# Kernel tuning notes

Measured on AMD Instinct MI355X. Metric: run time of the kernel, lower is better.

Reference implementation:

```python
import jax, jax.numpy as jnp
from jax import lax
import numpy as np

INPUT_SIZE = 2
HIDDEN_SIZE = 64
OUTPUT_SIZE = 2
SEQ_LEN = 1024
BATCH = 512


def setup_inputs() -> dict:
    key = jax.random.key(0)
    ks = jax.random.split(key, 7)
    H, I, O = HIDDEN_SIZE, INPUT_SIZE, OUTPUT_SIZE
    s = 1.0 / np.sqrt(H)  # PyTorch LSTM/Linear init scale
    x = jax.random.normal(ks[0], (SEQ_LEN, BATCH, I), dtype=jnp.float32)
    W_ih = jax.random.uniform(ks[1], (4 * H, I), minval=-s, maxval=s, dtype=jnp.float32)
    W_hh = jax.random.uniform(ks[2], (4 * H, H), minval=-s, maxval=s, dtype=jnp.float32)
    b_ih = jax.random.uniform(ks[3], (4 * H,), minval=-s, maxval=s, dtype=jnp.float32)
    b_hh = jax.random.uniform(ks[4], (4 * H,), minval=-s, maxval=s, dtype=jnp.float32)
    W_fc = jax.random.uniform(ks[5], (O, H), minval=-s, maxval=s, dtype=jnp.float32)
    b_fc = jax.random.uniform(ks[6], (O,), minval=-s, maxval=s, dtype=jnp.float32)
    return {"x": x, "W_ih": W_ih, "W_hh": W_hh, "b_ih": b_ih, "b_hh": b_hh,
            "W_fc": W_fc, "b_fc": b_fc}


def reference(x, W_ih, W_hh, b_ih, b_hh, W_fc, b_fc):
    # x: [T, B, I] (torch nn.LSTM default batch_first=False)
    T, B, _ = x.shape
    H = W_hh.shape[1]
    b = b_ih + b_hh  # [4H]

    def step(carry, xt):
        h, c = carry  # [B, H] each
        gates = xt @ W_ih.T + h @ W_hh.T + b  # [B, 4H]
        i, f, g, o = jnp.split(gates, 4, axis=-1)  # PyTorch gate order i,f,g,o
        i = jax.nn.sigmoid(i)
        f = jax.nn.sigmoid(f)
        g = jnp.tanh(g)
        o = jax.nn.sigmoid(o)
        c_new = f * c + i * g
        h_new = o * jnp.tanh(c_new)
        return (h_new, c_new), h_new

    h0 = jnp.zeros((B, H), dtype=x.dtype)
    c0 = jnp.zeros((B, H), dtype=x.dtype)
    _, hs = lax.scan(step, (h0, c0), x)  # hs: [T, B, H]

    # Faithful to torch: out[:, -1, :] with out shape [T, B, H] selects the
    # LAST BATCH element's hidden state at every timestep -> [T, H].
    last = hs[:, -1, :]
    return last @ W_fc.T + b_fc  # [T, O]
```

## Files before the change

kernel.cpp:

```cpp
#include <hip/hip_runtime.h>


typedef float f32x2 __attribute__((ext_vector_type(2)));

#define T_LEN 1024
#define BATCH 512
#define HID   64

__device__ __forceinline__ float fast_rcp(float x) {
    return __builtin_amdgcn_rcpf(x);
}
__device__ __forceinline__ float fast_sigmoid(float x) {
    return fast_rcp(1.0f + __expf(-x));
}
__device__ __forceinline__ float fast_tanh(float x) {
    return 1.0f - 2.0f * fast_rcp(__expf(2.0f * x) + 1.0f);
}

__global__ __launch_bounds__(64, 1)
void lstm_seq_kernel(const float* __restrict__ x,
                     const float* __restrict__ W_ih,
                     const float* __restrict__ W_hh,
                     const float* __restrict__ b_ih,
                     const float* __restrict__ b_hh,
                     const float* __restrict__ W_fc,
                     const float* __restrict__ b_fc,
                     float* __restrict__ out,
                     float* __restrict__ hist)
{
    __shared__ float xs[2 * T_LEN];

    const int lane = threadIdx.x;

    for (int j = 0; j < 16; ++j) {
        const int t = lane + 64 * j;
        const float2 v = *(const float2*)(x + (size_t)(t * BATCH + (BATCH - 1)) * 2);
        xs[2 * t]     = v.x;
        xs[2 * t + 1] = v.y;
    }

    f32x2 w0[32], w1[32], w2[32], w3[32];
    {
        const float4* r0 = (const float4*)(W_hh + (0 * HID + lane) * HID);
        const float4* r1 = (const float4*)(W_hh + (1 * HID + lane) * HID);
        const float4* r2 = (const float4*)(W_hh + (2 * HID + lane) * HID);
        const float4* r3 = (const float4*)(W_hh + (3 * HID + lane) * HID);
        #pragma unroll
        for (int k = 0; k < 16; ++k) {
            float4 v;
            v = r0[k]; w0[2*k] = (f32x2){v.x, v.y}; w0[2*k+1] = (f32x2){v.z, v.w};
            v = r1[k]; w1[2*k] = (f32x2){v.x, v.y}; w1[2*k+1] = (f32x2){v.z, v.w};
            v = r2[k]; w2[2*k] = (f32x2){v.x, v.y}; w2[2*k+1] = (f32x2){v.z, v.w};
            v = r3[k]; w3[2*k] = (f32x2){v.x, v.y}; w3[2*k+1] = (f32x2){v.z, v.w};
        }
    }
    const float wi00 = W_ih[(0 * HID + lane) * 2 + 0], wi01 = W_ih[(0 * HID + lane) * 2 + 1];
    const float wi10 = W_ih[(1 * HID + lane) * 2 + 0], wi11 = W_ih[(1 * HID + lane) * 2 + 1];
    const float wi20 = W_ih[(2 * HID + lane) * 2 + 0], wi21 = W_ih[(2 * HID + lane) * 2 + 1];
    const float wi30 = W_ih[(3 * HID + lane) * 2 + 0], wi31 = W_ih[(3 * HID + lane) * 2 + 1];
    const float bs0 = b_ih[0 * HID + lane] + b_hh[0 * HID + lane];
    const float bs1 = b_ih[1 * HID + lane] + b_hh[1 * HID + lane];
    const float bs2 = b_ih[2 * HID + lane] + b_hh[2 * HID + lane];
    const float bs3 = b_ih[3 * HID + lane] + b_hh[3 * HID + lane];

    float hval = 0.0f;
    float cval = 0.0f;

    for (int t = 0; t < T_LEN; ++t) {
        const float2 xv = *(const float2*)(xs + 2 * t);

        const int hb = __float_as_int(hval);
        f32x2 acc0 = (f32x2){0.0f, 0.0f};
        f32x2 acc1 = acc0, acc2 = acc0, acc3 = acc0;

        int hs[16];
        #pragma unroll
        for (int b = 0; b < 4; ++b) {
            #pragma unroll
            for (int k = 0; k < 16; ++k)
                hs[k] = __builtin_amdgcn_readlane(hb, 16 * b + k);
            __builtin_amdgcn_sched_barrier(0);
            #pragma unroll
            for (int p = 0; p < 8; ++p) {
                f32x2 hp;
                hp.x = __int_as_float(hs[2 * p]);
                hp.y = __int_as_float(hs[2 * p + 1]);
                const int i = 8 * b + p;
                acc0 += w0[i] * hp;
                acc1 += w1[i] * hp;
                acc2 += w2[i] * hp;
                acc3 += w3[i] * hp;
            }
        }

        float p0 = (acc0.x + acc0.y) + fmaf(wi00, xv.x, fmaf(wi01, xv.y, bs0));
        float p1 = (acc1.x + acc1.y) + fmaf(wi10, xv.x, fmaf(wi11, xv.y, bs1));
        float p2 = (acc2.x + acc2.y) + fmaf(wi20, xv.x, fmaf(wi21, xv.y, bs2));
        float p3 = (acc3.x + acc3.y) + fmaf(wi30, xv.x, fmaf(wi31, xv.y, bs3));

        const float gi = fast_sigmoid(p0);
        const float gf = fast_sigmoid(p1);
        const float gg = fast_tanh(p2);
        const float go = fast_sigmoid(p3);

        cval = fmaf(gf, cval, gi * gg);
        hval = go * fast_tanh(cval);

        hist[t * HID + lane] = hval;
    }

    for (int j = 0; j < 32; ++j) {
        const int idx = lane + 64 * j;
        const int t   = idx >> 1;
        const int o   = idx & 1;
        const float4* hv4 = (const float4*)(hist + t * HID);
        const float4* wv  = (const float4*)(W_fc + o * HID);
        float p0 = 0.f, p1 = 0.f, p2 = 0.f, p3 = 0.f;
        #pragma unroll
        for (int k = 0; k < HID / 4; ++k) {
            float4 h4 = hv4[k], w4 = wv[k];
            p0 = fmaf(h4.x, w4.x, p0);
            p1 = fmaf(h4.y, w4.y, p1);
            p2 = fmaf(h4.z, w4.z, p2);
            p3 = fmaf(h4.w, w4.w, p3);
        }
        out[idx] = b_fc[o] + ((p0 + p1) + (p2 + p3));
    }
}

extern "C" void kernel_launch(void* const* d_in, const int* in_sizes, int n_in,
                              void* d_out, int out_size, void* d_ws, size_t ws_size,
                              hipStream_t stream) {
    const float* x    = (const float*)d_in[0];
    const float* W_ih = (const float*)d_in[1];
    const float* W_hh = (const float*)d_in[2];
    const float* b_ih = (const float*)d_in[3];
    const float* b_hh = (const float*)d_in[4];
    const float* W_fc = (const float*)d_in[5];
    const float* b_fc = (const float*)d_in[6];
    float* out  = (float*)d_out;
    float* hist = (float*)d_ws;

    lstm_seq_kernel<<<dim3(1), dim3(64), 0, stream>>>(
        x, W_ih, W_hh, b_ih, b_hh, W_fc, b_fc, out, hist);
}
```

Baseline: 603.3 us.

## Compute LSTM recurrent matvec with f16 MFMA and LDS hidden-state exchange

Replaces the per-lane FP32 dot products, which broadcast h through readlane, with 16x16x32 f16 MFMA instructions. W_hh is converted to f16 A-fragments held in registers, and h is exchanged each step through a double-buffered LDS array. Gate results are scattered to LDS so each lane can read its four gates. This cuts the long chain of readlane and FMA instructions in the serial loop, but adds LDS round-trips, MFMA latency and f16 rounding of the weights and hidden state, which may hurt accuracy. Only column 0 of each MFMA output holds useful data, so most of the matrix throughput is wasted.

```diff
diff --git a/kernel.cpp b/kernel.cpp
--- a/kernel.cpp
+++ b/kernel.cpp
@@ -1,7 +1,9 @@
 #include <hip/hip_runtime.h>
 
 
-typedef float f32x2 __attribute__((ext_vector_type(2)));
+typedef _Float16 f16;
+typedef _Float16 f16x8 __attribute__((ext_vector_type(8)));
+typedef float    f32x4 __attribute__((ext_vector_type(4)));
 
 #define T_LEN 1024
 #define BATCH 512
@@ -28,9 +30,13 @@
                      float* __restrict__ out,
                      float* __restrict__ hist)
 {
-    __shared__ float xs[2 * T_LEN];
+    __shared__ __align__(16) float xs[2 * T_LEN];
+    __shared__ __align__(16) f16   hfrag[2][HID];
+    __shared__ __align__(16) float glds[2][4][72];
 
     const int lane = threadIdx.x;
+    const int qd   = lane >> 4;
+    const int cl   = lane & 15;
 
     for (int j = 0; j < 16; ++j) {
         const int t = lane + 64 * j;
@@ -39,86 +45,87 @@
         xs[2 * t + 1] = v.y;
     }
 
-    f32x2 w0[32], w1[32], w2[32], w3[32];
-    {
-        const float4* r0 = (const float4*)(W_hh + (0 * HID + lane) * HID);
-        const float4* r1 = (const float4*)(W_hh + (1 * HID + lane) * HID);
-        const float4* r2 = (const float4*)(W_hh + (2 * HID + lane) * HID);
-        const float4* r3 = (const float4*)(W_hh + (3 * HID + lane) * HID);
+    f16x8 afrag[16][2];
+    #pragma unroll
+    for (int i = 0; i < 16; ++i) {
         #pragma unroll
-        for (int k = 0; k < 16; ++k) {
-            float4 v;
-            v = r0[k]; w0[2*k] = (f32x2){v.x, v.y}; w0[2*k+1] = (f32x2){v.z, v.w};
-            v = r1[k]; w1[2*k] = (f32x2){v.x, v.y}; w1[2*k+1] = (f32x2){v.z, v.w};
-            v = r2[k]; w2[2*k] = (f32x2){v.x, v.y}; w2[2*k+1] = (f32x2){v.z, v.w};
-            v = r3[k]; w3[2*k] = (f32x2){v.x, v.y}; w3[2*k+1] = (f32x2){v.z, v.w};
+        for (int kk = 0; kk < 2; ++kk) {
+            const float* src = W_hh + (size_t)(16 * i + cl) * HID + 32 * kk + 8 * qd;
+            const float4 lo = *(const float4*)(src);
+            const float4 hi = *(const float4*)(src + 4);
+            f16x8 a;
+            a[0] = (f16)lo.x; a[1] = (f16)lo.y; a[2] = (f16)lo.z; a[3] = (f16)lo.w;
+            a[4] = (f16)hi.x; a[5] = (f16)hi.y; a[6] = (f16)hi.z; a[7] = (f16)hi.w;
+            afrag[i][kk] = a;
         }
     }
-    const float wi00 = W_ih[(0 * HID + lane) * 2 + 0], wi01 = W_ih[(0 * HID + lane) * 2 + 1];
-    const float wi10 = W_ih[(1 * HID + lane) * 2 + 0], wi11 = W_ih[(1 * HID + lane) * 2 + 1];
-    const float wi20 = W_ih[(2 * HID + lane) * 2 + 0], wi21 = W_ih[(2 * HID + lane) * 2 + 1];
-    const float wi30 = W_ih[(3 * HID + lane) * 2 + 0], wi31 = W_ih[(3 * HID + lane) * 2 + 1];
-    const float bs0 = b_ih[0 * HID + lane] + b_hh[0 * HID + lane];
-    const float bs1 = b_ih[1 * HID + lane] + b_hh[1 * HID + lane];
-    const float bs2 = b_ih[2 * HID + lane] + b_hh[2 * HID + lane];
-    const float bs3 = b_ih[3 * HID + lane] + b_hh[3 * HID + lane];
+
+    const float bs0 = b_ih[0*HID + lane] + b_hh[0*HID + lane];
+    const float bs1 = b_ih[1*HID + lane] + b_hh[1*HID + lane];
+    const float bs2 = b_ih[2*HID + lane] + b_hh[2*HID + lane];
+    const float bs3 = b_ih[3*HID + lane] + b_hh[3*HID + lane];
+    const float wiA0 = W_ih[(0*HID + lane)*2], wiB0 = W_ih[(0*HID + lane)*2 + 1];
+    const float wiA1 = W_ih[(1*HID + lane)*2], wiB1 = W_ih[(1*HID + lane)*2 + 1];
+    const float wiA2 = W_ih[(2*HID + lane)*2], wiB2 = W_ih[(2*HID + lane)*2 + 1];
+    const float wiA3 = W_ih[(3*HID + lane)*2], wiB3 = W_ih[(3*HID + lane)*2 + 1];
 
     float hval = 0.0f;
     float cval = 0.0f;
+    hfrag[0][lane] = (f16)0.0f;
+
+    const f32x4 zero = {0.0f, 0.0f, 0.0f, 0.0f};
 
     for (int t = 0; t < T_LEN; ++t) {
+        const int b = t & 1;
+
+        const char* hbase = (const char*)&hfrag[b][0];
+        const f16x8 bf0 = *(const f16x8*)(hbase + 16 * qd);
+        const f16x8 bf1 = *(const f16x8*)(hbase + 64 + 16 * qd);
+
         const float2 xv = *(const float2*)(xs + 2 * t);
 
-        const int hb = __float_as_int(hval);
-        f32x2 acc0 = (f32x2){0.0f, 0.0f};
-        f32x2 acc1 = acc0, acc2 = acc0, acc3 = acc0;
+        f32x4 acc[16];
+        #pragma unroll
+        for (int i = 0; i < 16; ++i)
+            acc[i] = __builtin_amdgcn_mfma_f32_16x16x32_f16(afrag[i][0], bf0, zero, 0, 0, 0);
+        #pragma unroll
+        for (int i = 0; i < 16; ++i)
+            acc[i] = __builtin_amdgcn_mfma_f32_16x16x32_f16(afrag[i][1], bf1, acc[i], 0, 0, 0);
 
-        int hs[16];
-        #pragma unroll
-        for (int b = 0; b < 4; ++b) {
+        const float xb0 = fmaf(wiA0, xv.x, fmaf(wiB0, xv.y, bs0));
+        const float xb1 = fmaf(wiA1, xv.x, fmaf(wiB1, xv.y, bs1));
+        const float xb2 = fmaf(wiA2, xv.x, fmaf(wiB2, xv.y, bs2));
+        const float xb3 = fmaf(wiA3, xv.x, fmaf(wiB3, xv.y, bs3));
+
+        if (cl == 0) {
             #pragma unroll
-            for (int k = 0; k < 16; ++k)
-                hs[k] = __builtin_amdgcn_readlane(hb, 16 * b + k);
-            __builtin_amdgcn_sched_barrier(0);
-            #pragma unroll
-            for (int p = 0; p < 8; ++p) {
-                f32x2 hp;
-                hp.x = __int_as_float(hs[2 * p]);
-                hp.y = __int_as_float(hs[2 * p + 1]);
-                const int i = 8 * b + p;
-                acc0 += w0[i] * hp;
-                acc1 += w1[i] * hp;
-                acc2 += w2[i] * hp;
-                acc3 += w3[i] * hp;
-            }
+            for (int i = 0; i < 16; ++i)
+                *(f32x4*)&glds[b][i >> 2][16 * (i & 3) + 4 * qd] = acc[i];
         }
 
-        float p0 = (acc0.x + acc0.y) + fmaf(wi00, xv.x, fmaf(wi01, xv.y, bs0));
-        float p1 = (acc1.x + acc1.y) + fmaf(wi10, xv.x, fmaf(wi11, xv.y, bs1));
-        float p2 = (acc2.x + acc2.y) + fmaf(wi20, xv.x, fmaf(wi21, xv.y, bs2));
-        float p3 = (acc3.x + acc3.y) + fmaf(wi30, xv.x, fmaf(wi31, xv.y, bs3));
-
-        const float gi = fast_sigmoid(p0);
-        const float gf = fast_sigmoid(p1);
-        const float gg = fast_tanh(p2);
-        const float go = fast_sigmoid(p3);
+        const float gi = fast_sigmoid(glds[b][0][lane] + xb0);
+        const float gf = fast_sigmoid(glds[b][1][lane] + xb1);
+        const float gg = fast_tanh   (glds[b][2][lane] + xb2);
+        const float go = fast_sigmoid(glds[b][3][lane] + xb3);
 
         cval = fmaf(gf, cval, gi * gg);
         hval = go * fast_tanh(cval);
 
         hist[t * HID + lane] = hval;
+
+        hfrag[(t + 1) & 1][lane] = (f16)hval;
     }
 
-    for (int j = 0; j < 32; ++j) {
-        const int idx = lane + 64 * j;
-        const int t   = idx >> 1;
+    for (int jj = 0; jj < 32; ++jj) {
+        const int idx = lane + 64 * jj;
+        const int tt  = idx >> 1;
         const int o   = idx & 1;
-        const float4* hv4 = (const float4*)(hist + t * HID);
+        const float4* hv4 = (const float4*)(hist + tt * HID);
         const float4* wv  = (const float4*)(W_fc + o * HID);
         float p0 = 0.f, p1 = 0.f, p2 = 0.f, p3 = 0.f;
         #pragma unroll
         for (int k = 0; k < HID / 4; ++k) {
-            float4 h4 = hv4[k], w4 = wv[k];
+            const float4 h4 = hv4[k], w4 = wv[k];
             p0 = fmaf(h4.x, w4.x, p0);
             p1 = fmaf(h4.y, w4.y, p1);
             p2 = fmaf(h4.z, w4.z, p2);
```

Result: slower. 800.6 us (+32.7%).
